# Optimization experiments

Measured on AMD Instinct MI355X. Metric: run time of the kernel, lower is better.

Reference implementation:

```python
import jax, jax.numpy as jnp
import numpy as np

N = 100000
E = 3200000
NEG_SLOPE = 0.2


def _gat(x, W, a_src, a_dst, b, src, dst, n):
    """PyG-style GATConv (eval mode, self-loops already appended to src/dst)."""
    H, C = a_src.shape
    h = (x @ W).reshape(n, H, C)                       # [N,H,C]
    es = jnp.einsum('nhc,hc->nh', h, a_src)            # per-node src logits
    ed = jnp.einsum('nhc,hc->nh', h, a_dst)
    e = jax.nn.leaky_relu(es[src] + ed[dst], NEG_SLOPE)  # [E,H]
    m = jax.ops.segment_max(e, dst, num_segments=n)    # stable softmax per dst
    ee = jnp.exp(e - m[dst])
    z = jax.ops.segment_sum(ee, dst, num_segments=n)
    alpha = ee / z[dst]                                # softmax over in-edges
    out = jax.ops.segment_sum(h[src] * alpha[:, :, None], dst, num_segments=n)
    return out.reshape(n, H * C) + b


def setup_inputs() -> dict:
    key = jax.random.key(0)
    ks = jax.random.split(key, 25)
    rn = lambda k, s, sc=0.1: jax.random.normal(k, s, dtype=jnp.float32) * sc
    return {
        'x1': rn(ks[0], (N, 8), 1.0),
        'x2': rn(ks[1], (N, 10), 1.0),
        'edge_index': jax.random.randint(ks[2], (2, E), 0, N, dtype=jnp.int32),
        'num_nodes': N,
        'Wq': rn(ks[3], (8, 16)), 'bq': rn(ks[4], (16,)),
        'Wk': rn(ks[5], (10, 16)), 'bk': rn(ks[6], (16,)),
        'Wv': rn(ks[7], (18, 16)), 'bv': rn(ks[8], (16,)),
        'W1': rn(ks[9], (16, 32)), 'a1s': rn(ks[10], (8, 4)), 'a1d': rn(ks[11], (8, 4)), 'b1': rn(ks[12], (32,)),
        'W2': rn(ks[13], (32, 16)), 'a2s': rn(ks[14], (4, 4)), 'a2d': rn(ks[15], (4, 4)), 'b2': rn(ks[16], (16,)),
        'W3': rn(ks[17], (16, 8)), 'a3s': rn(ks[18], (2, 4)), 'a3d': rn(ks[19], (2, 4)), 'b3': rn(ks[20], (8,)),
        'Wl2': rn(ks[21], (8, 1)),
    }


def reference(x1, x2, edge_index, num_nodes, Wq, bq, Wk, bk, Wv, bv,
              W1, a1s, a1d, b1, W2, a2s, a2d, b2, W3, a3s, a3d, b3, Wl2):
    n = num_nodes
    q = x1 @ Wq + bq                                   # [N,16]
    k = x2 @ Wk + bk                                   # [N,16]
    v = jnp.concatenate([x1, x2], axis=1) @ Wv + bv    # [N,16]
    score = jnp.sum(q * k, axis=1)                     # bmm(q[:,None,:], k[:,:,None]).squeeze()
    attw = jax.nn.softmax(score)[:, None]              # softmax over all nodes
    fused = attw * v                                   # [N,16]

    sl = jnp.arange(n, dtype=edge_index.dtype)         # GATConv adds self-loops
    src = jnp.concatenate([edge_index[0], sl])
    dst = jnp.concatenate([edge_index[1], sl])

    h1 = _gat(fused, W1, a1s, a1d, b1, src, dst, n)    # [N,32]
    h2 = _gat(h1, W2, a2s, a2d, b2, src, dst, n)       # [N,16]
    x4 = _gat(h2, W3, a3s, a3d, b3, src, dst, n)       # [N,8]; dropout=identity (eval)

    # Row-normalized adjacency (no self loops), expressed as O(E) segment ops.
    r, c = edge_index[0], edge_index[1]
    deg = jax.ops.segment_sum(jnp.ones_like(r, dtype=x4.dtype), r, num_segments=n)
    inv = jnp.where(deg > 0, 1.0 / deg, 0.0)[:, None]
    R3 = jax.ops.segment_sum(x4[c], r, num_segments=n) * inv  # Adj_norm @ x4
    local = jnp.sum(x4 * R3, axis=1, keepdims=True)    # sum_j Adjn[i,j]*(x4_i . x4_j)
    glob = R3 @ Wl2                                    # lin2 (no bias)
    return local + glob                                # [N,1]
```

## Files before the change

### kernel.cpp

```cpp
#include <hip/hip_runtime.h>

#define TPB 256
#define CAP 9216
#define EPB 4096
#define OFSW 784
#define GBPAD 784

typedef float f32x4 __attribute__((ext_vector_type(4)));
typedef float f32x2 __attribute__((ext_vector_type(2)));
typedef unsigned u32x4 __attribute__((ext_vector_type(4)));

__device__ __forceinline__ float lrelu(float x) { return x > 0.f ? x : 0.2f * x; }

__device__ __forceinline__ unsigned bfr(float x) {
  unsigned u = __float_as_uint(x);
  return (u + 0x7FFFu + ((u >> 16) & 1u)) >> 16;
}
__device__ __forceinline__ unsigned pk(float a, float b) { return bfr(a) | (bfr(b) << 16); }
__device__ __forceinline__ float ubf(unsigned us) { return __uint_as_float(us << 16); }

__global__ void __launch_bounds__(TPB) k_bucket(
    const int* __restrict__ ei, int E, int N,
    unsigned* __restrict__ items2, int* __restrict__ ofs)
{
  __shared__ int hist[1024];
  __shared__ int lofs[1024];
  __shared__ int scan_s[TPB];
  __shared__ unsigned stage[2 * EPB];
  int tid = threadIdx.x;
  for (int i = tid; i < 1024; i += TPB) hist[i] = 0;
  int s0 = blockIdx.x * EPB;
  int nE = min(EPB, E - s0);
  int sv[16], dv[16];
  __syncthreads();
#pragma unroll
  for (int k = 0; k < 4; k++) {
    int li = tid * 4 + k * TPB * 4;
    if (li + 3 < nE) {
      int4 s4 = *(const int4*)(ei + s0 + li);
      int4 d4 = *(const int4*)(ei + E + s0 + li);
      sv[k*4+0] = s4.x; sv[k*4+1] = s4.y; sv[k*4+2] = s4.z; sv[k*4+3] = s4.w;
      dv[k*4+0] = d4.x; dv[k*4+1] = d4.y; dv[k*4+2] = d4.z; dv[k*4+3] = d4.w;
#pragma unroll
      for (int j = 0; j < 4; j++) {
        atomicAdd(&hist[dv[k*4+j] >> 8], 1);
        atomicAdd(&hist[(N + sv[k*4+j]) >> 8], 1);
      }
    } else {
      for (int j = 0; j < 4; j++) {
        if (li + j < nE) {
          sv[k*4+j] = ei[s0 + li + j];
          dv[k*4+j] = ei[E + s0 + li + j];
          atomicAdd(&hist[dv[k*4+j] >> 8], 1);
          atomicAdd(&hist[(N + sv[k*4+j]) >> 8], 1);
        }
      }
    }
  }
  __syncthreads();
  int b0 = tid * 4;
  int c0 = hist[b0], c1 = hist[b0 + 1], c2 = hist[b0 + 2], c3 = hist[b0 + 3];
  int tsum = c0 + c1 + c2 + c3;
  scan_s[tid] = tsum;
  __syncthreads();
#pragma unroll
  for (int o = 1; o < TPB; o <<= 1) {
    int t = (tid >= o) ? scan_s[tid - o] : 0;
    __syncthreads();
    scan_s[tid] += t;
    __syncthreads();
  }
  int run = scan_s[tid] - tsum;
  int cs[4] = {c0, c1, c2, c3};
#pragma unroll
  for (int j = 0; j < 4; j++) {
    int b = b0 + j;
    lofs[b] = run;
    hist[b] = 0;
    run += cs[j];
  }
  __syncthreads();
#pragma unroll
  for (int k = 0; k < 16; k++) {
    int li = tid * 4 + (k >> 2) * TPB * 4 + (k & 3);
    if (li < nE) {
      int s = sv[k], d = dv[k];
      int b1 = d >> 8;
      int p1 = lofs[b1] + atomicAdd(&hist[b1], 1);
      stage[p1] = ((unsigned)(d & 255) << 24) | (unsigned)s;
      int k2 = N + s, b2 = k2 >> 8;
      int p2 = lofs[b2] + atomicAdd(&hist[b2], 1);
      stage[p2] = ((unsigned)(k2 & 255) << 24) | (unsigned)d;
    }
  }
  __syncthreads();
  int total = 2 * nE;
  size_t obase = (size_t)blockIdx.x * (2 * EPB);
  for (int idx = tid; idx < total; idx += TPB)
    __builtin_nontemporal_store(stage[idx], items2 + obase + idx);
  int orow = blockIdx.x * OFSW;
  for (int i = tid; i < OFSW; i += TPB)
    ofs[orow + i] = lofs[i];
}

__global__ void __launch_bounds__(TPB) k_t(
    const int* __restrict__ ofs, int* __restrict__ ofsT, int nB)
{
  __shared__ int tile[32][33];
  int lx = threadIdx.x & 31, ly = threadIdx.x >> 5;
  int b0 = blockIdx.y * 32, k0 = blockIdx.x * 32;
#pragma unroll
  for (int r = 0; r < 32; r += 8) {
    int b = b0 + ly + r, k = k0 + lx;
    tile[ly + r][lx] = (b < nB && k < OFSW) ? ofs[b * OFSW + k] : 0;
  }
  __syncthreads();
#pragma unroll
  for (int r = 0; r < 32; r += 8) {
    int k = k0 + ly + r, b = b0 + lx;
    if (k < OFSW && b < GBPAD) ofsT[k * GBPAD + b] = tile[lx][ly + r];
  }
}

__global__ void __launch_bounds__(TPB) k_csr2(
    const int* __restrict__ ofsT, const unsigned* __restrict__ items2, int nB,
    unsigned* __restrict__ items, int* __restrict__ rowptr, int* __restrict__ rowend, int n2)
{
  __shared__ unsigned stage[CAP];
  __shared__ int cnt_s[TPB], scan_s[TPB], off_s[TPB];
  int tid = threadIdx.x, k = blockIdx.x;
  cnt_s[tid] = 0;
  int o0[4], cl[4];
  int tsum = 0;
#pragma unroll
  for (int m = 0; m < 4; m++) {
    int b = tid + m * TPB;
    if (b < nB) {
      int a0 = ofsT[(size_t)k * GBPAD + b];
      int a1 = ofsT[(size_t)(k + 1) * GBPAD + b];
      o0[m] = a0; cl[m] = a1 - a0;
    } else { o0[m] = 0; cl[m] = 0; }
    tsum += cl[m];
  }
  scan_s[tid] = tsum;
  __syncthreads();
#pragma unroll
  for (int o = 1; o < TPB; o <<= 1) {
    int t = (tid >= o) ? scan_s[tid - o] : 0;
    __syncthreads();
    scan_s[tid] += t;
    __syncthreads();
  }
  int cnt = min(scan_s[TPB - 1], CAP);
  int dst = scan_s[tid] - tsum;
#pragma unroll
  for (int m = 0; m < 4; m++) {
    int b = tid + m * TPB;
    const unsigned* src = items2 + (size_t)b * (2 * EPB) + o0[m];
    int c = cl[m];
    int j = 0;
    int head = (4 - (o0[m] & 3)) & 3; if (head > c) head = c;
    for (; j < head; j++) { int p = dst + j; if (p < CAP) stage[p] = src[j]; }
    for (; j + 3 < c; j += 4) {
      u32x4 v = *(const u32x4*)(src + j);
      int p = dst + j;
      if (p + 3 < CAP) {
        stage[p] = v.x; stage[p+1] = v.y; stage[p+2] = v.z; stage[p+3] = v.w;
      } else {
        if (p < CAP) stage[p] = v.x;
        if (p+1 < CAP) stage[p+1] = v.y;
        if (p+2 < CAP) stage[p+2] = v.z;
        if (p+3 < CAP) stage[p+3] = v.w;
      }
    }
    for (; j < c; j++) { int p = dst + j; if (p < CAP) stage[p] = src[j]; }
    dst += c;
  }
  __syncthreads();
  for (int i = tid; i < cnt; i += TPB) atomicAdd(&cnt_s[stage[i] >> 24], 1);
  __syncthreads();
  int v = cnt_s[tid];
  scan_s[tid] = v;
  __syncthreads();
#pragma unroll
  for (int o = 1; o < TPB; o <<= 1) {
    int t = (tid >= o) ? scan_s[tid - o] : 0;
    __syncthreads();
    scan_s[tid] += t;
    __syncthreads();
  }
  int excl = scan_s[tid] - v;
  off_s[tid] = excl;
  size_t bbase = (size_t)k * CAP;
  int g = k * 256 + tid;
  if (g < n2) { rowptr[g] = (int)bbase + excl; rowend[g] = (int)bbase + excl + v; }
  cnt_s[tid] = 0;
  __syncthreads();
  for (int i = tid; i < cnt; i += TPB) {
    unsigned u = stage[i];
    int kk = u >> 24;
    int r = atomicAdd(&cnt_s[kk], 1);
    items[bbase + off_s[kk] + r] = u & 0xFFFFFFu;
  }
}


__global__ void __launch_bounds__(TPB) k_score(
    const float* __restrict__ x1, const float* __restrict__ x2,
    const float* __restrict__ Wq, const float* __restrict__ bq,
    const float* __restrict__ Wk, const float* __restrict__ bk,
    float* __restrict__ escore, float* __restrict__ sumexp, int N)
{
  __shared__ float sWq[128], sWk[160], sbq[16], sbk[16];
  for (int i = threadIdx.x; i < 128; i += TPB) sWq[i] = Wq[i];
  for (int i = threadIdx.x; i < 160; i += TPB) sWk[i] = Wk[i];
  if (threadIdx.x < 16) { sbq[threadIdx.x] = bq[threadIdx.x]; sbk[threadIdx.x] = bk[threadIdx.x]; }
  __syncthreads();
  int n = blockIdx.x * TPB + threadIdx.x;
  float e = 0.f;
  if (n < N) {
    float a[8], b[10];
#pragma unroll
    for (int i = 0; i < 8; i++) a[i] = x1[n*8 + i];
#pragma unroll
    for (int i = 0; i < 10; i++) b[i] = x2[n*10 + i];
    float score = 0.f;
#pragma unroll
    for (int j = 0; j < 16; j++) {
      float q = sbq[j], k = sbk[j];
#pragma unroll
      for (int i = 0; i < 8; i++) q += a[i] * sWq[i*16 + j];
#pragma unroll
      for (int i = 0; i < 10; i++) k += b[i] * sWk[i*16 + j];
      score += q * k;
    }
    e = __expf(score);
    escore[n] = e;
  }
  float v = e;
#pragma unroll
  for (int off = 32; off > 0; off >>= 1) v += __shfl_down(v, off);
  __shared__ float red[TPB / 64];
  if ((threadIdx.x & 63) == 0) red[threadIdx.x >> 6] = v;
  __syncthreads();
  if (threadIdx.x == 0) {
    float s = 0.f;
#pragma unroll
    for (int w = 0; w < TPB / 64; w++) s += red[w];
    atomicAdd(sumexp, s);
  }
}

__global__ void __launch_bounds__(TPB) k_A1(
    const float* __restrict__ x1, const float* __restrict__ x2,
    const float* __restrict__ Wv, const float* __restrict__ bv,
    const float* __restrict__ W1, const float* __restrict__ a1s, const float* __restrict__ a1d,
    const float* __restrict__ escore, const float* __restrict__ sumexp,
    unsigned* __restrict__ rec1a, unsigned* __restrict__ rec1b,
    float* __restrict__ ed, int N)
{
  __shared__ float sWv[288], sbv[16], sW1[512], sas[32], sad[32];
  for (int i = threadIdx.x; i < 288; i += TPB) sWv[i] = Wv[i];
  for (int i = threadIdx.x; i < 512; i += TPB) sW1[i] = W1[i];
  if (threadIdx.x < 16) sbv[threadIdx.x] = bv[threadIdx.x];
  if (threadIdx.x < 32) { sas[threadIdx.x] = a1s[threadIdx.x]; sad[threadIdx.x] = a1d[threadIdx.x]; }
  __syncthreads();
  int n = blockIdx.x * TPB + threadIdx.x;
  if (n >= N) return;
  float w = escore[n] / sumexp[0];
  float f[16];
  {
    float a[8], b[10];
#pragma unroll
    for (int i = 0; i < 8; i++) a[i] = x1[n*8 + i];
#pragma unroll
    for (int i = 0; i < 10; i++) b[i] = x2[n*10 + i];
#pragma unroll
    for (int j = 0; j < 16; j++) {
      float v = sbv[j];
#pragma unroll
      for (int i = 0; i < 8; i++) v += a[i] * sWv[i*16 + j];
#pragma unroll
      for (int i = 0; i < 10; i++) v += b[i] * sWv[(8 + i)*16 + j];
      f[j] = w * v;
    }
  }
  float hr[32], esv[8], edv[8];
#pragma unroll
  for (int j = 0; j < 32; j++) {
    float s = 0.f;
#pragma unroll
    for (int i = 0; i < 16; i++) s += f[i] * sW1[i*32 + j];
    hr[j] = s;
  }
#pragma unroll
  for (int hh = 0; hh < 8; hh++) {
    float s = 0.f, d = 0.f;
#pragma unroll
    for (int c = 0; c < 4; c++) { s += hr[hh*4+c]*sas[hh*4+c]; d += hr[hh*4+c]*sad[hh*4+c]; }
    esv[hh] = s; edv[hh] = d;
  }
  unsigned* ra = rec1a + (size_t)n*16;
  unsigned* rb = rec1b + (size_t)n*16;
#pragma unroll
  for (int hh = 0; hh < 4; hh++) {
    u32x4 qa = { __float_as_uint(esv[hh]),
                 pk(hr[hh*4+0], hr[hh*4+1]), pk(hr[hh*4+2], hr[hh*4+3]), 0u };
    u32x4 qb = { __float_as_uint(esv[4+hh]),
                 pk(hr[16+hh*4+0], hr[16+hh*4+1]), pk(hr[16+hh*4+2], hr[16+hh*4+3]), 0u };
    __builtin_nontemporal_store(qa, (u32x4*)(ra + hh*4));
    __builtin_nontemporal_store(qb, (u32x4*)(rb + hh*4));
  }
  f32x4 e0 = {edv[0], edv[1], edv[2], edv[3]};
  f32x4 e1 = {edv[4], edv[5], edv[6], edv[7]};
  *(f32x4*)(ed + n*8)     = e0;
  *(f32x4*)(ed + n*8 + 4) = e1;
}

__global__ void __launch_bounds__(TPB) k_B2(
    const float* __restrict__ W2, const float* __restrict__ a2s, const float* __restrict__ a2d,
    const float* __restrict__ X,
    unsigned* __restrict__ rec2, float* __restrict__ ed, int N)
{
  __shared__ float sW[512], sas[16], sad[16];
  for (int i = threadIdx.x; i < 512; i += TPB) sW[i] = W2[i];
  if (threadIdx.x < 16) { sas[threadIdx.x] = a2s[threadIdx.x]; sad[threadIdx.x] = a2d[threadIdx.x]; }
  __syncthreads();
  int n = blockIdx.x * TPB + threadIdx.x;
  if (n >= N) return;
  float Xr[32];
#pragma unroll
  for (int i = 0; i < 8; i++) {
    f32x4 t = __builtin_nontemporal_load((const f32x4*)(X + n*32) + i);
    Xr[i*4+0] = t.x; Xr[i*4+1] = t.y; Xr[i*4+2] = t.z; Xr[i*4+3] = t.w;
  }
  float hr[16];
#pragma unroll
  for (int j = 0; j < 16; j++) {
    float s = 0.f;
#pragma unroll
    for (int f = 0; f < 32; f++) s += Xr[f] * sW[f*16 + j];
    hr[j] = s;
  }
  unsigned* r = rec2 + (size_t)n*16;
#pragma unroll
  for (int hh = 0; hh < 4; hh++) {
    float s = 0.f, d = 0.f;
#pragma unroll
    for (int c = 0; c < 4; c++) { s += hr[hh*4+c]*sas[hh*4+c]; d += hr[hh*4+c]*sad[hh*4+c]; }
    u32x4 q = { __float_as_uint(s),
                pk(hr[hh*4+0], hr[hh*4+1]), pk(hr[hh*4+2], hr[hh*4+3]), 0u };
    __builtin_nontemporal_store(q, (u32x4*)(r + hh*4));
    ed[n*8 + hh] = d;
  }
}

__global__ void __launch_bounds__(TPB) k_B3(
    const float* __restrict__ W3, const float* __restrict__ a3s, const float* __restrict__ a3d,
    const float* __restrict__ X3,
    unsigned* __restrict__ rec3, float* __restrict__ ed, int N)
{
  __shared__ float sW[128], sas[8], sad[8];
  for (int i = threadIdx.x; i < 128; i += TPB) sW[i] = W3[i];
  if (threadIdx.x < 8) { sas[threadIdx.x] = a3s[threadIdx.x]; sad[threadIdx.x] = a3d[threadIdx.x]; }
  __syncthreads();
  int n = blockIdx.x * TPB + threadIdx.x;
  if (n >= N) return;
  float Xr[16];
#pragma unroll
  for (int i = 0; i < 4; i++) {
    f32x4 t = __builtin_nontemporal_load((const f32x4*)(X3 + n*16) + i);
    Xr[i*4+0] = t.x; Xr[i*4+1] = t.y; Xr[i*4+2] = t.z; Xr[i*4+3] = t.w;
  }
  float hr[8];
#pragma unroll
  for (int j = 0; j < 8; j++) {
    float s = 0.f;
#pragma unroll
    for (int f = 0; f < 16; f++) s += Xr[f] * sW[f*8 + j];
    hr[j] = s;
  }
  unsigned* r = rec3 + (size_t)n*8;
#pragma unroll
  for (int hh = 0; hh < 2; hh++) {
    float s = 0.f, d = 0.f;
#pragma unroll
    for (int c = 0; c < 4; c++) { s += hr[hh*4+c]*sas[hh*4+c]; d += hr[hh*4+c]*sad[hh*4+c]; }
    u32x4 q = { __float_as_uint(s),
                pk(hr[hh*4+0], hr[hh*4+1]), pk(hr[hh*4+2], hr[hh*4+3]), 0u };
    __builtin_nontemporal_store(q, (u32x4*)(r + hh*4));
    ed[n*8 + hh] = d;
  }
}

template<int OS, int HOFF>
__global__ void __launch_bounds__(TPB) k_gat4(
    const int* __restrict__ rowptr, const int* __restrict__ rowend, const int* __restrict__ col,
    const unsigned* __restrict__ rec, const float* __restrict__ ed,
    const float* __restrict__ bias, float* __restrict__ out, int N)
{
  int wave = (blockIdx.x * TPB + threadIdx.x) >> 6;
  if (wave >= N) return;
  int lane = threadIdx.x & 63;
  int hh = lane & 3, j = lane >> 2;
  int d = wave;
  int e0 = rowptr[d], deg = rowend[d] - e0;
  float edv = ed[d*8 + HOFF + hh];
  float z = 0.f;
  f32x4 acc = {0.f, 0.f, 0.f, 0.f};
  for (int t = j; t <= deg; t += 16) {
    int s = (t == deg) ? d : __builtin_nontemporal_load(col + e0 + t);
    u32x4 q = *(const u32x4*)(rec + (size_t)s*16 + hh*4);
    float w = __expf(lrelu(__uint_as_float(q.x) + edv));
    z += w;
    acc.x += w * ubf(q.y & 0xFFFFu); acc.y += w * ubf(q.y >> 16);
    acc.z += w * ubf(q.z & 0xFFFFu); acc.w += w * ubf(q.z >> 16);
  }
#pragma unroll
  for (int m = 4; m < 64; m <<= 1) {
    z += __shfl_xor(z, m);
    acc.x += __shfl_xor(acc.x, m); acc.y += __shfl_xor(acc.y, m);
    acc.z += __shfl_xor(acc.z, m); acc.w += __shfl_xor(acc.w, m);
  }
  if (j == 0) {
    float inv = 1.f / z;
    const f32x4 bb = *(const f32x4*)(bias + (HOFF + hh)*4);
    f32x4 o = { acc.x*inv + bb.x, acc.y*inv + bb.y, acc.z*inv + bb.z, acc.w*inv + bb.w };
    __builtin_nontemporal_store(o, (f32x4*)(out + (size_t)d*OS + (HOFF + hh)*4));
  }
}

__global__ void __launch_bounds__(TPB) k_gat3(
    const int* __restrict__ rowptr, const int* __restrict__ rowend, const int* __restrict__ col,
    const unsigned* __restrict__ rec, const float* __restrict__ ed,
    const float* __restrict__ b3, float* __restrict__ x4, int N)
{
  int wave = (blockIdx.x * TPB + threadIdx.x) >> 6;
  if (wave >= N) return;
  int lane = threadIdx.x & 63;
  int hh = lane & 1, j = lane >> 1;
  int d = wave;
  int e0 = rowptr[d], deg = rowend[d] - e0;
  float edv = ed[d*8 + hh];
  float z = 0.f;
  f32x4 acc = {0.f, 0.f, 0.f, 0.f};
  for (int t = j; t <= deg; t += 32) {
    int s = (t == deg) ? d : __builtin_nontemporal_load(col + e0 + t);
    u32x4 q = *(const u32x4*)(rec + (size_t)s*8 + hh*4);
    float w = __expf(lrelu(__uint_as_float(q.x) + edv));
    z += w;
    acc.x += w * ubf(q.y & 0xFFFFu); acc.y += w * ubf(q.y >> 16);
    acc.z += w * ubf(q.z & 0xFFFFu); acc.w += w * ubf(q.z >> 16);
  }
#pragma unroll
  for (int m = 2; m < 64; m <<= 1) {
    z += __shfl_xor(z, m);
    acc.x += __shfl_xor(acc.x, m); acc.y += __shfl_xor(acc.y, m);
    acc.z += __shfl_xor(acc.z, m); acc.w += __shfl_xor(acc.w, m);
  }
  if (j == 0) {
    float inv = 1.f / z;
    const f32x4 bb = *(const f32x4*)(b3 + hh*4);
    f32x4 o = { acc.x*inv + bb.x, acc.y*inv + bb.y, acc.z*inv + bb.z, acc.w*inv + bb.w };
    __builtin_nontemporal_store(o, (f32x4*)(x4 + d*8 + hh*4));
  }
}

__global__ void __launch_bounds__(TPB) k_adj_final(
    const int* __restrict__ rowptr, const int* __restrict__ rowend, const int* __restrict__ col,
    const float* __restrict__ x4, const float* __restrict__ Wl2,
    float* __restrict__ out, int N)
{
  __shared__ float sW[8];
  if (threadIdx.x < 8) sW[threadIdx.x] = Wl2[threadIdx.x];
  __syncthreads();
  int wave = (blockIdx.x * TPB + threadIdx.x) >> 6;
  if (wave >= N) return;
  int lane = threadIdx.x & 63;
  int q = lane & 1, j = lane >> 1;
  int r = wave;
  int e0 = rowptr[N + r], deg = rowend[N + r] - e0;
  f32x4 acc = {0.f, 0.f, 0.f, 0.f};
  for (int t = j; t < deg; t += 32) {
    int c = __builtin_nontemporal_load(col + e0 + t);
    f32x4 xv = *(const f32x4*)(x4 + c*8 + q*4);
    acc.x += xv.x; acc.y += xv.y; acc.z += xv.z; acc.w += xv.w;
  }
#pragma unroll
  for (int m = 2; m < 64; m <<= 1) {
    acc.x += __shfl_xor(acc.x, m); acc.y += __shfl_xor(acc.y, m);
    acc.z += __shfl_xor(acc.z, m); acc.w += __shfl_xor(acc.w, m);
  }
  float part = 0.f;
  if (j == 0) {
    float inv = deg > 0 ? 1.f / (float)deg : 0.f;
    f32x4 R = { acc.x*inv, acc.y*inv, acc.z*inv, acc.w*inv };
    f32x4 xo = *(const f32x4*)(x4 + r*8 + q*4);
    part = xo.x*R.x + xo.y*R.y + xo.z*R.z + xo.w*R.w
         + R.x*sW[q*4+0] + R.y*sW[q*4+1] + R.z*sW[q*4+2] + R.w*sW[q*4+3];
  }
  part += __shfl_xor(part, 1);
  if (lane == 0) out[r] = part;
}

extern "C" void kernel_launch(void* const* d_in, const int* in_sizes, int n_in,
                              void* d_out, int out_size, void* d_ws, size_t ws_size,
                              hipStream_t stream)
{
  const float* x1  = (const float*)d_in[0];
  const float* x2  = (const float*)d_in[1];
  const int*   ei  = (const int*)d_in[2];
  const float* Wq  = (const float*)d_in[4];
  const float* bq  = (const float*)d_in[5];
  const float* Wk  = (const float*)d_in[6];
  const float* bk  = (const float*)d_in[7];
  const float* Wv  = (const float*)d_in[8];
  const float* bv  = (const float*)d_in[9];
  const float* W1  = (const float*)d_in[10];
  const float* a1s = (const float*)d_in[11];
  const float* a1d = (const float*)d_in[12];
  const float* b1  = (const float*)d_in[13];
  const float* W2  = (const float*)d_in[14];
  const float* a2s = (const float*)d_in[15];
  const float* a2d = (const float*)d_in[16];
  const float* b2  = (const float*)d_in[17];
  const float* W3  = (const float*)d_in[18];
  const float* a3s = (const float*)d_in[19];
  const float* a3d = (const float*)d_in[20];
  const float* b3  = (const float*)d_in[21];
  const float* Wl2 = (const float*)d_in[22];

  int N = in_sizes[0] / 8;
  int E = in_sizes[2] / 2;
  int n2 = 2 * N;
  int NB = (n2 + 255) >> 8;
  int gB = (E + EPB - 1) / EPB;

  float* sumexp = (float*)d_ws;
  int* rowptr   = (int*)(sumexp + 16);
  int* rowend   = rowptr + (size_t)n2;
  unsigned* itemsCSR = (unsigned*)(rowend + (size_t)n2);
  unsigned* regionA  = itemsCSR + (size_t)NB * CAP;
  unsigned* items2 = regionA;
  int* ofs  = (int*)(items2 + (size_t)gB * (2 * EPB));
  int* ofsT = ofs + (size_t)gB * OFSW;
  size_t raSize = (size_t)gB * (2 * EPB + OFSW) + (size_t)OFSW * GBPAD;
  unsigned* rec1a = regionA;
  unsigned* rec1b = rec1a + 16ull*N;
  unsigned* rec2  = rec1b + 16ull*N;
  unsigned* rec3  = rec2 + 16ull*N;
  float* ed       = (float*)(rec3 + 8ull*N);
  float* escore   = ed + 8ull*N;
  float* X        = (float*)(regionA + raSize);
  float* X3 = X;
  float* x4 = (float*)rec1b;

  int gN = (N + TPB - 1) / TPB;
  int g64 = (int)(((long long)N * 64 + TPB - 1) / TPB);

  (void)hipMemsetAsync(sumexp, 0, 16 * sizeof(float), stream);

  k_bucket<<<gB, TPB, 0, stream>>>(ei, E, N, items2, ofs);
  dim3 gt((OFSW + 31) / 32, (gB + 31) / 32);
  k_t<<<gt, TPB, 0, stream>>>(ofs, ofsT, gB);
  k_csr2<<<NB, TPB, 0, stream>>>(ofsT, items2, gB, itemsCSR, rowptr, rowend, n2);
  int* colv = (int*)itemsCSR;

  k_score<<<gN, TPB, 0, stream>>>(x1, x2, Wq, bq, Wk, bk, escore, sumexp, N);
  k_A1<<<gN, TPB, 0, stream>>>(x1, x2, Wv, bv, W1, a1s, a1d, escore, sumexp, rec1a, rec1b, ed, N);

  k_gat4<32, 0><<<g64, TPB, 0, stream>>>(rowptr, rowend, colv, rec1a, ed, b1, X, N);
  k_gat4<32, 4><<<g64, TPB, 0, stream>>>(rowptr, rowend, colv, rec1b, ed, b1, X, N);
  k_B2<<<gN, TPB, 0, stream>>>(W2, a2s, a2d, X, rec2, ed, N);
  k_gat4<16, 0><<<g64, TPB, 0, stream>>>(rowptr, rowend, colv, rec2, ed, b2, X3, N);
  k_B3<<<gN, TPB, 0, stream>>>(W3, a3s, a3d, X3, rec3, ed, N);
  k_gat3<<<g64, TPB, 0, stream>>>(rowptr, rowend, colv, rec3, ed, b3, x4, N);

  k_adj_final<<<g64, TPB, 0, stream>>>(rowptr, rowend, colv, x4, Wl2, (float*)d_out, N);
}
```

Before: 482.8 us.

## Merge two half-head GAT layer-1 passes into one 8-head pass

Layer-1 aggregation used to run two passes over the CSR, each covering four heads and reading a 64-byte per-node record. Now one kernel covers all eight heads from a single 128-byte record, and each wave handles 8 edges per step instead of 16. The goal is to read the column indices and row pointers once instead of twice and to drop one kernel launch, at the price of less edge-level parallelism per wave on high-degree rows.

```diff
diff --git a/kernel.cpp b/kernel.cpp
--- a/kernel.cpp
+++ b/kernel.cpp
@@ -256,8 +256,7 @@
     const float* __restrict__ Wv, const float* __restrict__ bv,
     const float* __restrict__ W1, const float* __restrict__ a1s, const float* __restrict__ a1d,
     const float* __restrict__ escore, const float* __restrict__ sumexp,
-    unsigned* __restrict__ rec1a, unsigned* __restrict__ rec1b,
-    float* __restrict__ ed, int N)
+    unsigned* __restrict__ rec1, float* __restrict__ ed, int N)
 {
   __shared__ float sWv[288], sbv[16], sW1[512], sas[32], sad[32];
   for (int i = threadIdx.x; i < 288; i += TPB) sWv[i] = Wv[i];
@@ -300,16 +299,12 @@
     for (int c = 0; c < 4; c++) { s += hr[hh*4+c]*sas[hh*4+c]; d += hr[hh*4+c]*sad[hh*4+c]; }
     esv[hh] = s; edv[hh] = d;
   }
-  unsigned* ra = rec1a + (size_t)n*16;
-  unsigned* rb = rec1b + (size_t)n*16;
-#pragma unroll
-  for (int hh = 0; hh < 4; hh++) {
-    u32x4 qa = { __float_as_uint(esv[hh]),
-                 pk(hr[hh*4+0], hr[hh*4+1]), pk(hr[hh*4+2], hr[hh*4+3]), 0u };
-    u32x4 qb = { __float_as_uint(esv[4+hh]),
-                 pk(hr[16+hh*4+0], hr[16+hh*4+1]), pk(hr[16+hh*4+2], hr[16+hh*4+3]), 0u };
-    __builtin_nontemporal_store(qa, (u32x4*)(ra + hh*4));
-    __builtin_nontemporal_store(qb, (u32x4*)(rb + hh*4));
+  unsigned* r = rec1 + (size_t)n*32;
+#pragma unroll
+  for (int hh = 0; hh < 8; hh++) {
+    u32x4 q = { __float_as_uint(esv[hh]),
+                pk(hr[hh*4+0], hr[hh*4+1]), pk(hr[hh*4+2], hr[hh*4+3]), 0u };
+    __builtin_nontemporal_store(q, (u32x4*)(r + hh*4));
   }
   f32x4 e0 = {edv[0], edv[1], edv[2], edv[3]};
   f32x4 e1 = {edv[4], edv[5], edv[6], edv[7]};
@@ -393,8 +388,43 @@
   }
 }
 
-template<int OS, int HOFF>
-__global__ void __launch_bounds__(TPB) k_gat4(
+__global__ void __launch_bounds__(TPB) k_gat1(
+    const int* __restrict__ rowptr, const int* __restrict__ rowend, const int* __restrict__ col,
+    const unsigned* __restrict__ rec, const float* __restrict__ ed,
+    const float* __restrict__ bias, float* __restrict__ out, int N)
+{
+  int wave = (blockIdx.x * TPB + threadIdx.x) >> 6;
+  if (wave >= N) return;
+  int lane = threadIdx.x & 63;
+  int hh = lane & 7, j = lane >> 3;
+  int d = wave;
+  int e0 = rowptr[d], deg = rowend[d] - e0;
+  float edv = ed[d*8 + hh];
+  float z = 0.f;
+  f32x4 acc = {0.f, 0.f, 0.f, 0.f};
+  for (int t = j; t <= deg; t += 8) {
+    int s = (t == deg) ? d : __builtin_nontemporal_load(col + e0 + t);
+    u32x4 q = *(const u32x4*)(rec + (size_t)s*32 + hh*4);
+    float w = __expf(lrelu(__uint_as_float(q.x) + edv));
+    z += w;
+    acc.x += w * ubf(q.y & 0xFFFFu); acc.y += w * ubf(q.y >> 16);
+    acc.z += w * ubf(q.z & 0xFFFFu); acc.w += w * ubf(q.z >> 16);
+  }
+#pragma unroll
+  for (int m = 8; m < 64; m <<= 1) {
+    z += __shfl_xor(z, m);
+    acc.x += __shfl_xor(acc.x, m); acc.y += __shfl_xor(acc.y, m);
+    acc.z += __shfl_xor(acc.z, m); acc.w += __shfl_xor(acc.w, m);
+  }
+  if (j == 0) {
+    float inv = 1.f / z;
+    const f32x4 bb = *(const f32x4*)(bias + hh*4);
+    f32x4 o = { acc.x*inv + bb.x, acc.y*inv + bb.y, acc.z*inv + bb.z, acc.w*inv + bb.w };
+    __builtin_nontemporal_store(o, (f32x4*)(out + (size_t)d*32 + hh*4));
+  }
+}
+
+__global__ void __launch_bounds__(TPB) k_gat2(
     const int* __restrict__ rowptr, const int* __restrict__ rowend, const int* __restrict__ col,
     const unsigned* __restrict__ rec, const float* __restrict__ ed,
     const float* __restrict__ bias, float* __restrict__ out, int N)
@@ -405,7 +435,7 @@
   int hh = lane & 3, j = lane >> 2;
   int d = wave;
   int e0 = rowptr[d], deg = rowend[d] - e0;
-  float edv = ed[d*8 + HOFF + hh];
+  float edv = ed[d*8 + hh];
   float z = 0.f;
   f32x4 acc = {0.f, 0.f, 0.f, 0.f};
   for (int t = j; t <= deg; t += 16) {
@@ -424,9 +454,9 @@
   }
   if (j == 0) {
     float inv = 1.f / z;
-    const f32x4 bb = *(const f32x4*)(bias + (HOFF + hh)*4);
+    const f32x4 bb = *(const f32x4*)(bias + hh*4);
     f32x4 o = { acc.x*inv + bb.x, acc.y*inv + bb.y, acc.z*inv + bb.z, acc.w*inv + bb.w };
-    __builtin_nontemporal_store(o, (f32x4*)(out + (size_t)d*OS + (HOFF + hh)*4));
+    __builtin_nontemporal_store(o, (f32x4*)(out + (size_t)d*16 + hh*4));
   }
 }
 
@@ -545,15 +575,14 @@
   int* ofs  = (int*)(items2 + (size_t)gB * (2 * EPB));
   int* ofsT = ofs + (size_t)gB * OFSW;
   size_t raSize = (size_t)gB * (2 * EPB + OFSW) + (size_t)OFSW * GBPAD;
-  unsigned* rec1a = regionA;
-  unsigned* rec1b = rec1a + 16ull*N;
-  unsigned* rec2  = rec1b + 16ull*N;
+  unsigned* rec1  = regionA;
+  unsigned* rec2  = rec1 + 32ull*N;
   unsigned* rec3  = rec2 + 16ull*N;
   float* ed       = (float*)(rec3 + 8ull*N);
   float* escore   = ed + 8ull*N;
   float* X        = (float*)(regionA + raSize);
   float* X3 = X;
-  float* x4 = (float*)rec1b;
+  float* x4 = (float*)rec1;
 
   int gN = (N + TPB - 1) / TPB;
   int g64 = (int)(((long long)N * 64 + TPB - 1) / TPB);
@@ -567,12 +596,11 @@
   int* colv = (int*)itemsCSR;
 
   k_score<<<gN, TPB, 0, stream>>>(x1, x2, Wq, bq, Wk, bk, escore, sumexp, N);
-  k_A1<<<gN, TPB, 0, stream>>>(x1, x2, Wv, bv, W1, a1s, a1d, escore, sumexp, rec1a, rec1b, ed, N);
-
-  k_gat4<32, 0><<<g64, TPB, 0, stream>>>(rowptr, rowend, colv, rec1a, ed, b1, X, N);
-  k_gat4<32, 4><<<g64, TPB, 0, stream>>>(rowptr, rowend, colv, rec1b, ed, b1, X, N);
+  k_A1<<<gN, TPB, 0, stream>>>(x1, x2, Wv, bv, W1, a1s, a1d, escore, sumexp, rec1, ed, N);
+
+  k_gat1<<<g64, TPB, 0, stream>>>(rowptr, rowend, colv, rec1, ed, b1, X, N);
   k_B2<<<gN, TPB, 0, stream>>>(W2, a2s, a2d, X, rec2, ed, N);
-  k_gat4<16, 0><<<g64, TPB, 0, stream>>>(rowptr, rowend, colv, rec2, ed, b2, X3, N);
+  k_gat2<<<g64, TPB, 0, stream>>>(rowptr, rowend, colv, rec2, ed, b2, X3, N);
   k_B3<<<gN, TPB, 0, stream>>>(W3, a3s, a3d, X3, rec3, ed, N);
   k_gat3<<<g64, TPB, 0, stream>>>(rowptr, rowend, colv, rec3, ed, b3, x4, N);
 
```

Result: no change. 475.3 us (-1.5%).
